# Performance work log

Hardware: AMD Instinct MI355X
Metric: run time of the kernel (lower is better)

The kernel has to match this reference:

```python
import jax, jax.numpy as jnp
import numpy as np

N, F_IN, D, H = 4096, 128, 128, 4  # nodes, in_features, n_hidden(out_features), n_heads


def setup_inputs() -> dict:
    key = jax.random.key(0)
    ks = jax.random.split(key, 5)
    h = jax.random.normal(ks[0], (N, F_IN), jnp.float32)
    adj_mat = jax.random.randint(ks[1], (N, N), 0, 2, jnp.int32)
    pos = jax.random.normal(ks[2], (N, 3), jnp.float32)
    # xavier_normal-ish scales
    W = jax.random.normal(ks[3], (F_IN, D * H), jnp.float32) * (2.0 / (F_IN + D * H)) ** 0.5
    a = jax.random.normal(ks[4], (H, 2 * D, 1), jnp.float32) * (2.0 / (2 * D + 1)) ** 0.5
    ln_gamma = jnp.ones((D,), jnp.float32)
    ln_beta = jnp.zeros((D,), jnp.float32)
    return dict(h=h, adj_mat=adj_mat, pos=pos, W=W, a=a, ln_gamma=ln_gamma, ln_beta=ln_beta)


def reference(h, adj_mat, pos, W, a, ln_gamma, ln_beta):
    n = h.shape[0]
    ht = (h @ W).reshape(n, H, D).transpose(1, 0, 2)          # (H, N, D)
    src = ht @ a[:, :D, :]                                    # (H, N, 1)
    tgt = ht @ a[:, D:, :]                                    # (H, N, 1)
    diff = pos[:, None, :] - pos[None, :, :]                  # (N, N, 3) rel_pos
    dist = jnp.sqrt(jnp.sum(diff * diff, axis=-1))            # (N, N) cdist p=2
    e = src + jnp.transpose(tgt, (0, 2, 1)) - dist[None]      # (H, N, N)
    e = jnp.where(e > 0, e, 0.2 * e)                          # LeakyReLU(0.2)
    e = jnp.where(adj_mat[None] > 0, e, jnp.float32(-9e15))   # connectivity mask
    attention = jax.nn.softmax(e, axis=-1)                    # (H, N, N)
    h_prime = attention @ ht                                  # (H, N, D)
    hm = jnp.mean(h_prime, axis=0)                            # (N, D) mean over heads
    mu = jnp.mean(hm, axis=-1, keepdims=True)
    var = jnp.var(hm, axis=-1, keepdims=True)
    hn = (hm - mu) / jnp.sqrt(var + 1e-5) * ln_gamma + ln_beta  # LayerNorm
    h_out = h + hn
    att_mean = jnp.mean(attention, axis=0)                    # (N, N)
    delta = jnp.einsum('ij,ijk->ik', att_mean, diff)          # (N, 3)
    pos_out = pos + delta
    return h_out, pos_out
```

## Files before the change

kernel.cpp:

```cpp
#include <hip/hip_runtime.h>
#include <hip/hip_bf16.h>
#include <math.h>

#define NN 4096
#define HH 4

typedef _Float16 h2 __attribute__((ext_vector_type(2)));
typedef _Float16 h4 __attribute__((ext_vector_type(4)));
typedef _Float16 h8 __attribute__((ext_vector_type(8)));
typedef float f4 __attribute__((ext_vector_type(4)));

static __device__ __forceinline__ h2 cvt2(float a, float b) {
  return __builtin_bit_cast(h2, __builtin_amdgcn_cvt_pkrtz(a, b));
}

__global__ __launch_bounds__(512) void k_htgemm(const float* __restrict__ h,
                                                const float* __restrict__ W,
                                                const float* __restrict__ a,
                                                const float* __restrict__ pos,
                                                _Float16* __restrict__ vfrag,
                                                _Float16* __restrict__ posfrag,
                                                float* __restrict__ src,
                                                float* __restrict__ tgt) {
  __shared__ float hs[16][128];
  __shared__ float red[8][16][2];
  const int jt = blockIdx.x;
  const int i0 = jt * 16;
  const int tid = threadIdx.x;
  for (int idx = tid; idx < 16 * 128; idx += 512)
    hs[idx >> 7][idx & 127] = h[(i0 + (idx >> 7)) * 128 + (idx & 127)];
  __syncthreads();
  const int c = tid;
  float acc[16];
#pragma unroll
  for (int r = 0; r < 16; ++r) acc[r] = 0.f;
  for (int k = 0; k < 128; ++k) {
    const float w = W[k * 512 + c];
#pragma unroll
    for (int r = 0; r < 16; ++r) acc[r] = fmaf(hs[r][k], w, acc[r]);
  }
  const int hc = c >> 7, d = c & 127;
  _Float16* vb = vfrag + ((size_t)(hc * 256 + jt) * 64) * 32 + (d >> 4) * 4;
#pragma unroll
  for (int rg = 0; rg < 4; ++rg) {
    h4 v;
    v.x = (_Float16)acc[rg * 4 + 0];
    v.y = (_Float16)acc[rg * 4 + 1];
    v.z = (_Float16)acc[rg * 4 + 2];
    v.w = (_Float16)acc[rg * 4 + 3];
    *(h4*)(vb + ((d & 15) + 16 * rg) * 32) = v;
  }
  const float av = a[hc * 256 + d];
  const float bvv = a[hc * 256 + 128 + d];
  float sv[16], tv[16];
#pragma unroll
  for (int r = 0; r < 16; ++r) { sv[r] = acc[r] * av; tv[r] = acc[r] * bvv; }
#pragma unroll
  for (int off = 32; off >= 1; off >>= 1) {
#pragma unroll
    for (int r = 0; r < 16; ++r) {
      sv[r] += __shfl_xor(sv[r], off, 64);
      tv[r] += __shfl_xor(tv[r], off, 64);
    }
  }
  const int w = tid >> 6;
  if ((tid & 63) == 0) {
#pragma unroll
    for (int r = 0; r < 16; ++r) { red[w][r][0] = sv[r]; red[w][r][1] = tv[r]; }
  }
  if (tid < 64) {
    const int rg = tid >> 4, n = tid & 15;
    h4 pv;
#pragma unroll
    for (int e = 0; e < 4; ++e) {
      const int j = i0 + rg * 4 + e;
      pv[e] = (_Float16)(n < 3 ? pos[j * 3 + n] : (n == 3 ? 1.f : 0.f));
    }
    *(h4*)(posfrag + (size_t)(jt * 64 + tid) * 4) = pv;
  }
  __syncthreads();
  if (tid < 128) {
    const int h2_ = tid >> 5, k = tid & 31, r = k >> 1, st = k & 1;
    const float vsum = red[h2_ * 2][r][st] + red[h2_ * 2 + 1][r][st];
    (st ? tgt : src)[h2_ * NN + i0 + r] = vsum;
  }
}

#define JROW 1036
#define SMEM_BYTES 67584

__global__ __launch_bounds__(512, 3) void k_attn(
    const _Float16* __restrict__ vfrag, const _Float16* __restrict__ posfrag,
    const int* __restrict__ adj, const float* __restrict__ pos,
    const float* __restrict__ src, const float* __restrict__ tgt,
    __hip_bfloat16* __restrict__ hp_part, __hip_bfloat16* __restrict__ ppart) {
  __shared__ __attribute__((aligned(16))) unsigned char smem[SMEM_BYTES];
  _Float16* dist16 = (_Float16*)smem;

  const int tid = threadIdx.x;
  const int bid = (int)blockIdx.x;
  const int ib = bid >> 2, jhb = bid & 3;
  const int i0 = ib * 32;
  const int jb = jhb * 1024;

  {
    const int si = tid >> 4;
    const int jc = (tid & 15) * 4;
    const float pix = pos[(i0 + si) * 3 + 0];
    const float piy = pos[(i0 + si) * 3 + 1];
    const float piz = pos[(i0 + si) * 3 + 2];
    const int* adjp = adj + (size_t)(i0 + si) * NN + jb + jc;
    const float* posj = pos + (size_t)(jb + jc) * 3;
#pragma unroll
    for (int cc = 0; cc < 16; ++cc) {
      const int4 av = *(const int4*)(adjp + cc * 64);
      const float4 p0 = *(const float4*)(posj + cc * 192 + 0);
      const float4 p1 = *(const float4*)(posj + cc * 192 + 4);
      const float4 p2 = *(const float4*)(posj + cc * 192 + 8);
      float dx, dy, dz;
      h4 dd;
      dx = pix - p0.x; dy = piy - p0.y; dz = piz - p0.z;
      dd.x = (_Float16)(av.x > 0 ? sqrtf(dx * dx + dy * dy + dz * dz) : 3e4f);
      dx = pix - p0.w; dy = piy - p1.x; dz = piz - p1.y;
      dd.y = (_Float16)(av.y > 0 ? sqrtf(dx * dx + dy * dy + dz * dz) : 3e4f);
      dx = pix - p1.z; dy = piy - p1.w; dz = piz - p2.x;
      dd.z = (_Float16)(av.z > 0 ? sqrtf(dx * dx + dy * dy + dz * dz) : 3e4f);
      dx = pix - p2.y; dy = piy - p2.z; dz = piz - p2.w;
      dd.w = (_Float16)(av.w > 0 ? sqrtf(dx * dx + dy * dy + dz * dz) : 3e4f);
      *(h4*)(dist16 + si * JROW + jc + cc * 64) = dd;
    }
  }
  __syncthreads();

  const int w = tid >> 6, lane = tid & 63;
  const int hh = w & 3, kp = w >> 2;
  const int il = lane & 15, kg = lane >> 4;

  const float srcv0 = src[hh * NN + i0 + il];
  const float srcv1 = src[hh * NN + i0 + 16 + il];

  f4 acc[2][8];
#pragma unroll
  for (int mp = 0; mp < 2; ++mp)
#pragma unroll
    for (int dt = 0; dt < 8; ++dt) acc[mp][dt] = (f4){0.f, 0.f, 0.f, 0.f};
  f4 pacc0 = (f4){0.f, 0.f, 0.f, 0.f};
  f4 pacc1 = (f4){0.f, 0.f, 0.f, 0.f};

  const int jt0 = (jb >> 4) + kp;
  const _Float16* vbase = vfrag + ((size_t)(hh * 256 + jt0) * 64 + lane) * 32;
  const _Float16* pbase = posfrag + (size_t)(jt0 * 64 + lane) * 4;
  const float* tbase = tgt + hh * NN + jb + kp * 16 + kg * 4;
  const _Float16* ddbase = dist16 + il * JROW + kp * 16 + kg * 4;

#define RELOAD(V01, V23, V45, V67, PF, TT, T)                \
  {                                                          \
    const _Float16* vfn = vbase + (size_t)(T) * 4096;        \
    V01 = *(const h8*)(vfn);                                 \
    V23 = *(const h8*)(vfn + 8);                             \
    V45 = *(const h8*)(vfn + 16);                            \
    V67 = *(const h8*)(vfn + 24);                            \
    PF = *(const h4*)(pbase + (T) * 512);                    \
    TT = *(const float4*)(tbase + (T) * 32);                 \
  }

#define BODYM(V01, V23, V45, V67, PF, TT, T)                                    \
  {                                                                             \
    const int toff = 2 * (T) * 16;                                              \
    const h4 dd0 = *(const h4*)(ddbase + toff);                                 \
    const h4 dd1 = *(const h4*)(ddbase + 16 * JROW + toff);                     \
    float e0 = (srcv0 + TT.x) - (float)dd0.x;                                   \
    float e1 = (srcv0 + TT.y) - (float)dd0.y;                                   \
    float e2 = (srcv0 + TT.z) - (float)dd0.z;                                   \
    float e3 = (srcv0 + TT.w) - (float)dd0.w;                                   \
    e0 = fmaxf(e0, 0.2f * e0); e1 = fmaxf(e1, 0.2f * e1);                       \
    e2 = fmaxf(e2, 0.2f * e2); e3 = fmaxf(e3, 0.2f * e3);                       \
    const h2 lo0 = cvt2(__expf(e0), __expf(e1));                                \
    const h2 hi0 = cvt2(__expf(e2), __expf(e3));                                \
    const h4 af0 = __builtin_shufflevector(lo0, hi0, 0, 1, 2, 3);               \
    float f0 = (srcv1 + TT.x) - (float)dd1.x;                                   \
    float f1 = (srcv1 + TT.y) - (float)dd1.y;                                   \
    float f2 = (srcv1 + TT.z) - (float)dd1.z;                                   \
    float f3 = (srcv1 + TT.w) - (float)dd1.w;                                   \
    f0 = fmaxf(f0, 0.2f * f0); f1 = fmaxf(f1, 0.2f * f1);                       \
    f2 = fmaxf(f2, 0.2f * f2); f3 = fmaxf(f3, 0.2f * f3);                       \
    const h2 lo1 = cvt2(__expf(f0), __expf(f1));                                \
    const h2 hi1 = cvt2(__expf(f2), __expf(f3));                                \
    const h4 af1 = __builtin_shufflevector(lo1, hi1, 0, 1, 2, 3);               \
    h4 vfj[8];                                                                  \
    vfj[0] = __builtin_shufflevector(V01, V01, 0, 1, 2, 3);                     \
    vfj[1] = __builtin_shufflevector(V01, V01, 4, 5, 6, 7);                     \
    vfj[2] = __builtin_shufflevector(V23, V23, 0, 1, 2, 3);                     \
    vfj[3] = __builtin_shufflevector(V23, V23, 4, 5, 6, 7);                     \
    vfj[4] = __builtin_shufflevector(V45, V45, 0, 1, 2, 3);                     \
    vfj[5] = __builtin_shufflevector(V45, V45, 4, 5, 6, 7);                     \
    vfj[6] = __builtin_shufflevector(V67, V67, 0, 1, 2, 3);                     \
    vfj[7] = __builtin_shufflevector(V67, V67, 4, 5, 6, 7);                     \
    __builtin_amdgcn_s_setprio(1);                                              \
    _Pragma("unroll") for (int dt = 0; dt < 8; ++dt)                            \
        acc[0][dt] = __builtin_amdgcn_mfma_f32_16x16x16f16(af0, vfj[dt],        \
                                                           acc[0][dt], 0, 0, 0);\
    pacc0 = __builtin_amdgcn_mfma_f32_16x16x16f16(af0, PF, pacc0, 0, 0, 0);     \
    _Pragma("unroll") for (int dt = 0; dt < 8; ++dt)                            \
        acc[1][dt] = __builtin_amdgcn_mfma_f32_16x16x16f16(af1, vfj[dt],        \
                                                           acc[1][dt], 0, 0, 0);\
    pacc1 = __builtin_amdgcn_mfma_f32_16x16x16f16(af1, PF, pacc1, 0, 0, 0);     \
    __builtin_amdgcn_s_setprio(0);                                              \
  }

  h8 A01, A23, A45, A67; h4 Apf; float4 Att;
  h8 B01, B23, B45, B67; h4 Bpf; float4 Btt;
  RELOAD(A01, A23, A45, A67, Apf, Att, 0);
  RELOAD(B01, B23, B45, B67, Bpf, Btt, 1);

#pragma unroll 1
  for (int t2 = 0; t2 < 15; ++t2) {
    const int t = t2 * 2;
    BODYM(A01, A23, A45, A67, Apf, Att, t);
    RELOAD(A01, A23, A45, A67, Apf, Att, t + 2);
    BODYM(B01, B23, B45, B67, Bpf, Btt, t + 1);
    RELOAD(B01, B23, B45, B67, Bpf, Btt, t + 3);
  }
  BODYM(A01, A23, A45, A67, Apf, Att, 30);
  BODYM(B01, B23, B45, B67, Bpf, Btt, 31);

#undef RELOAD
#undef BODYM

  __syncthreads();
  float* eps = (float*)smem;
  float* pacc_s = (float*)(smem + 65536);
  if (kp == 1) {
#pragma unroll
    for (int mp = 0; mp < 2; ++mp)
#pragma unroll
      for (int dt = 0; dt < 8; ++dt)
#pragma unroll
        for (int r = 0; r < 4; ++r)
          eps[(hh * 32 + mp * 16 + kg * 4 + r) * 128 + dt * 16 + il] = acc[mp][dt][r];
    if (il < 4) {
#pragma unroll
      for (int r = 0; r < 4; ++r) {
        pacc_s[(hh * 32 + kg * 4 + r) * 4 + il] = pacc0[r];
        pacc_s[(hh * 32 + 16 + kg * 4 + r) * 4 + il] = pacc1[r];
      }
    }
  }
  __syncthreads();
  if (kp == 0) {
    __hip_bfloat16* hpb = hp_part + ((size_t)(jhb * 4 + hh) * NN + i0) * 128;
#pragma unroll
    for (int mp = 0; mp < 2; ++mp)
#pragma unroll
      for (int dt = 0; dt < 8; ++dt)
#pragma unroll
        for (int r = 0; r < 4; ++r) {
          const int ii = mp * 16 + kg * 4 + r;
          const float s = (mp == 0 ? acc[0][dt][r] : acc[1][dt][r]) +
                          eps[(hh * 32 + ii) * 128 + dt * 16 + il];
          hpb[(size_t)ii * 128 + dt * 16 + il] = __float2bfloat16(s);
        }
    if (il < 4) {
#pragma unroll
      for (int r = 0; r < 4; ++r) {
        const float s0 = pacc0[r] + pacc_s[(hh * 32 + kg * 4 + r) * 4 + il];
        ppart[((size_t)(jhb * 4 + hh) * NN + i0 + kg * 4 + r) * 4 + il] =
            __float2bfloat16(s0);
        const float s1 = pacc1[r] + pacc_s[(hh * 32 + 16 + kg * 4 + r) * 4 + il];
        ppart[((size_t)(jhb * 4 + hh) * NN + i0 + 16 + kg * 4 + r) * 4 + il] =
            __float2bfloat16(s1);
      }
    }
  }
}

__global__ __launch_bounds__(128) void k_finish(
    const __hip_bfloat16* __restrict__ hp_part,
    const __hip_bfloat16* __restrict__ ppart, const float* __restrict__ hin,
    const float* __restrict__ pos, const float* __restrict__ gamma,
    const float* __restrict__ beta, float* __restrict__ hout,
    float* __restrict__ out_pos) {
  __shared__ float red[2][2];
  const int i = blockIdx.x, d = threadIdx.x;
  float Li[4];
  float v = 0.f;
#pragma unroll
  for (int hx = 0; hx < 4; ++hx) {
    float L = 0.f, hv = 0.f;
#pragma unroll
    for (int jh = 0; jh < 4; ++jh) {
      L += __bfloat162float(ppart[((size_t)(jh * 4 + hx) * NN + i) * 4 + 3]);
      hv += __bfloat162float(hp_part[((size_t)(jh * 4 + hx) * NN + i) * 128 + d]);
    }
    Li[hx] = 1.f / L;
    v += hv * Li[hx];
  }
  v *= 0.25f;
  float s = v, sq = v * v;
#pragma unroll
  for (int off = 32; off >= 1; off >>= 1) {
    s += __shfl_xor(s, off, 64);
    sq += __shfl_xor(sq, off, 64);
  }
  const int wv = d >> 6;
  if ((d & 63) == 0) { red[wv][0] = s; red[wv][1] = sq; }
  __syncthreads();
  s = red[0][0] + red[1][0];
  sq = red[0][1] + red[1][1];
  const float mu = s * (1.f / 128.f);
  const float var = sq * (1.f / 128.f) - mu * mu;
  const float hn = (v - mu) * rsqrtf(var + 1e-5f) * gamma[d] + beta[d];
  hout[i * 128 + d] = hin[i * 128 + d] + hn;
  if (d < 3) {
    float sp = 0.f;
#pragma unroll
    for (int hx = 0; hx < 4; ++hx) {
      float pv = 0.f;
#pragma unroll
      for (int jh = 0; jh < 4; ++jh)
        pv += __bfloat162float(ppart[((size_t)(jh * 4 + hx) * NN + i) * 4 + d]);
      sp += pv * Li[hx];
    }
    out_pos[i * 3 + d] = 2.f * pos[i * 3 + d] - 0.25f * sp;
  }
}

extern "C" void kernel_launch(void* const* d_in, const int* in_sizes, int n_in,
                              void* d_out, int out_size, void* d_ws, size_t ws_size,
                              hipStream_t stream) {
  const float* h     = (const float*)d_in[0];
  const int*   adj   = (const int*)d_in[1];
  const float* pos   = (const float*)d_in[2];
  const float* W     = (const float*)d_in[3];
  const float* a     = (const float*)d_in[4];
  const float* gamma = (const float*)d_in[5];
  const float* beta  = (const float*)d_in[6];
  float* out = (float*)d_out;

  unsigned char* ws = (unsigned char*)d_ws;
  _Float16* vfrag   = (_Float16*)ws;
  _Float16* posfrag = (_Float16*)(ws + 4194304);
  float* src        = (float*)(ws + 4194304 + 131072);
  float* tgt        = (float*)(ws + 4194304 + 131072 + 65536);
  __hip_bfloat16* hp_part =
      (__hip_bfloat16*)(ws + 4194304 + 131072 + 131072);
  __hip_bfloat16* ppart =
      (__hip_bfloat16*)(ws + 4194304 + 131072 + 131072 + 16777216);

  k_htgemm<<<NN / 16, 512, 0, stream>>>(h, W, a, pos, vfrag, posfrag, src, tgt);
  k_attn<<<(NN / 32) * 4, 512, 0, stream>>>(vfrag, posfrag, adj, pos, src, tgt,
                                            hp_part, ppart);
  k_finish<<<NN, 128, 0, stream>>>(hp_part, ppart, h, pos, gamma, beta, out,
                                   out + NN * 128);
}
```

Measured before the change: 107.8 us.

## Use exp2 with log2e prescaling, single-buffer prefetch loop, raise occupancy to 4

Multiplies src/tgt and the distances by log2(e) ahead of time so the inner loop can call the hardware exp2 directly instead of __expf, which saves a multiply per element. The two-register-set double-buffered loop becomes a single-stage prefetch loop that also prefetches the LDS distance values, which cuts register pressure. The launch bound rises from 3 to 4 blocks per CU. The masked-entry sentinel changes from 3e4 to 4e4, and the extra occupancy depends on LDS use and registers fitting; otherwise the lighter prefetch may hide less memory latency.

```diff
diff --git a/kernel.cpp b/kernel.cpp
--- a/kernel.cpp
+++ b/kernel.cpp
@@ -4,6 +4,7 @@
 
 #define NN 4096
 #define HH 4
+#define LOG2E 1.44269504f
 
 typedef _Float16 h2 __attribute__((ext_vector_type(2)));
 typedef _Float16 h4 __attribute__((ext_vector_type(4)));
@@ -13,6 +14,12 @@
 static __device__ __forceinline__ h2 cvt2(float a, float b) {
   return __builtin_bit_cast(h2, __builtin_amdgcn_cvt_pkrtz(a, b));
 }
+
+#if __has_builtin(__builtin_amdgcn_exp2f)
+#define EXP2(x) __builtin_amdgcn_exp2f(x)
+#else
+#define EXP2(x) exp2f(x)
+#endif
 
 __global__ __launch_bounds__(512) void k_htgemm(const float* __restrict__ h,
                                                 const float* __restrict__ W,
@@ -81,7 +88,7 @@
   __syncthreads();
   if (tid < 128) {
     const int h2_ = tid >> 5, k = tid & 31, r = k >> 1, st = k & 1;
-    const float vsum = red[h2_ * 2][r][st] + red[h2_ * 2 + 1][r][st];
+    const float vsum = (red[h2_ * 2][r][st] + red[h2_ * 2 + 1][r][st]) * LOG2E;
     (st ? tgt : src)[h2_ * NN + i0 + r] = vsum;
   }
 }
@@ -89,7 +96,7 @@
 #define JROW 1036
 #define SMEM_BYTES 67584
 
-__global__ __launch_bounds__(512, 3) void k_attn(
+__global__ __launch_bounds__(512, 4) void k_attn(
     const _Float16* __restrict__ vfrag, const _Float16* __restrict__ posfrag,
     const int* __restrict__ adj, const float* __restrict__ pos,
     const float* __restrict__ src, const float* __restrict__ tgt,
@@ -120,13 +127,13 @@
       float dx, dy, dz;
       h4 dd;
       dx = pix - p0.x; dy = piy - p0.y; dz = piz - p0.z;
-      dd.x = (_Float16)(av.x > 0 ? sqrtf(dx * dx + dy * dy + dz * dz) : 3e4f);
+      dd.x = (_Float16)(av.x > 0 ? sqrtf(dx * dx + dy * dy + dz * dz) * LOG2E : 4e4f);
       dx = pix - p0.w; dy = piy - p1.x; dz = piz - p1.y;
-      dd.y = (_Float16)(av.y > 0 ? sqrtf(dx * dx + dy * dy + dz * dz) : 3e4f);
+      dd.y = (_Float16)(av.y > 0 ? sqrtf(dx * dx + dy * dy + dz * dz) * LOG2E : 4e4f);
       dx = pix - p1.z; dy = piy - p1.w; dz = piz - p2.x;
-      dd.z = (_Float16)(av.z > 0 ? sqrtf(dx * dx + dy * dy + dz * dz) : 3e4f);
+      dd.z = (_Float16)(av.z > 0 ? sqrtf(dx * dx + dy * dy + dz * dz) * LOG2E : 4e4f);
       dx = pix - p2.y; dy = piy - p2.z; dz = piz - p2.w;
-      dd.w = (_Float16)(av.w > 0 ? sqrtf(dx * dx + dy * dy + dz * dz) : 3e4f);
+      dd.w = (_Float16)(av.w > 0 ? sqrtf(dx * dx + dy * dy + dz * dz) * LOG2E : 4e4f);
       *(h4*)(dist16 + si * JROW + jc + cc * 64) = dd;
     }
   }
@@ -153,79 +160,70 @@
   const float* tbase = tgt + hh * NN + jb + kp * 16 + kg * 4;
   const _Float16* ddbase = dist16 + il * JROW + kp * 16 + kg * 4;
 
-#define RELOAD(V01, V23, V45, V67, PF, TT, T)                \
-  {                                                          \
-    const _Float16* vfn = vbase + (size_t)(T) * 4096;        \
-    V01 = *(const h8*)(vfn);                                 \
-    V23 = *(const h8*)(vfn + 8);                             \
-    V45 = *(const h8*)(vfn + 16);                            \
-    V67 = *(const h8*)(vfn + 24);                            \
-    PF = *(const h4*)(pbase + (T) * 512);                    \
-    TT = *(const float4*)(tbase + (T) * 32);                 \
-  }
-
-#define BODYM(V01, V23, V45, V67, PF, TT, T)                                    \
-  {                                                                             \
-    const int toff = 2 * (T) * 16;                                              \
-    const h4 dd0 = *(const h4*)(ddbase + toff);                                 \
-    const h4 dd1 = *(const h4*)(ddbase + 16 * JROW + toff);                     \
-    float e0 = (srcv0 + TT.x) - (float)dd0.x;                                   \
-    float e1 = (srcv0 + TT.y) - (float)dd0.y;                                   \
-    float e2 = (srcv0 + TT.z) - (float)dd0.z;                                   \
-    float e3 = (srcv0 + TT.w) - (float)dd0.w;                                   \
-    e0 = fmaxf(e0, 0.2f * e0); e1 = fmaxf(e1, 0.2f * e1);                       \
-    e2 = fmaxf(e2, 0.2f * e2); e3 = fmaxf(e3, 0.2f * e3);                       \
-    const h2 lo0 = cvt2(__expf(e0), __expf(e1));                                \
-    const h2 hi0 = cvt2(__expf(e2), __expf(e3));                                \
-    const h4 af0 = __builtin_shufflevector(lo0, hi0, 0, 1, 2, 3);               \
-    float f0 = (srcv1 + TT.x) - (float)dd1.x;                                   \
-    float f1 = (srcv1 + TT.y) - (float)dd1.y;                                   \
-    float f2 = (srcv1 + TT.z) - (float)dd1.z;                                   \
-    float f3 = (srcv1 + TT.w) - (float)dd1.w;                                   \
-    f0 = fmaxf(f0, 0.2f * f0); f1 = fmaxf(f1, 0.2f * f1);                       \
-    f2 = fmaxf(f2, 0.2f * f2); f3 = fmaxf(f3, 0.2f * f3);                       \
-    const h2 lo1 = cvt2(__expf(f0), __expf(f1));                                \
-    const h2 hi1 = cvt2(__expf(f2), __expf(f3));                                \
-    const h4 af1 = __builtin_shufflevector(lo1, hi1, 0, 1, 2, 3);               \
-    h4 vfj[8];                                                                  \
-    vfj[0] = __builtin_shufflevector(V01, V01, 0, 1, 2, 3);                     \
-    vfj[1] = __builtin_shufflevector(V01, V01, 4, 5, 6, 7);                     \
-    vfj[2] = __builtin_shufflevector(V23, V23, 0, 1, 2, 3);                     \
-    vfj[3] = __builtin_shufflevector(V23, V23, 4, 5, 6, 7);                     \
-    vfj[4] = __builtin_shufflevector(V45, V45, 0, 1, 2, 3);                     \
-    vfj[5] = __builtin_shufflevector(V45, V45, 4, 5, 6, 7);                     \
-    vfj[6] = __builtin_shufflevector(V67, V67, 0, 1, 2, 3);                     \
-    vfj[7] = __builtin_shufflevector(V67, V67, 4, 5, 6, 7);                     \
-    __builtin_amdgcn_s_setprio(1);                                              \
-    _Pragma("unroll") for (int dt = 0; dt < 8; ++dt)                            \
-        acc[0][dt] = __builtin_amdgcn_mfma_f32_16x16x16f16(af0, vfj[dt],        \
-                                                           acc[0][dt], 0, 0, 0);\
-    pacc0 = __builtin_amdgcn_mfma_f32_16x16x16f16(af0, PF, pacc0, 0, 0, 0);     \
-    _Pragma("unroll") for (int dt = 0; dt < 8; ++dt)                            \
-        acc[1][dt] = __builtin_amdgcn_mfma_f32_16x16x16f16(af1, vfj[dt],        \
-                                                           acc[1][dt], 0, 0, 0);\
-    pacc1 = __builtin_amdgcn_mfma_f32_16x16x16f16(af1, PF, pacc1, 0, 0, 0);     \
-    __builtin_amdgcn_s_setprio(0);                                              \
-  }
-
-  h8 A01, A23, A45, A67; h4 Apf; float4 Att;
-  h8 B01, B23, B45, B67; h4 Bpf; float4 Btt;
-  RELOAD(A01, A23, A45, A67, Apf, Att, 0);
-  RELOAD(B01, B23, B45, B67, Bpf, Btt, 1);
-
-#pragma unroll 1
-  for (int t2 = 0; t2 < 15; ++t2) {
-    const int t = t2 * 2;
-    BODYM(A01, A23, A45, A67, Apf, Att, t);
-    RELOAD(A01, A23, A45, A67, Apf, Att, t + 2);
-    BODYM(B01, B23, B45, B67, Bpf, Btt, t + 1);
-    RELOAD(B01, B23, B45, B67, Bpf, Btt, t + 3);
-  }
-  BODYM(A01, A23, A45, A67, Apf, Att, 30);
-  BODYM(B01, B23, B45, B67, Bpf, Btt, 31);
-
-#undef RELOAD
-#undef BODYM
+  h8 n01 = *(const h8*)(vbase);
+  h8 n23 = *(const h8*)(vbase + 8);
+  h8 n45 = *(const h8*)(vbase + 16);
+  h8 n67 = *(const h8*)(vbase + 24);
+  h4 npf = *(const h4*)(pbase);
+  float4 ntt = *(const float4*)(tbase);
+  h4 ndd0 = *(const h4*)(ddbase);
+  h4 ndd1 = *(const h4*)(ddbase + 16 * JROW);
+
+#pragma unroll 2
+  for (int t = 0; t < 32; ++t) {
+    const h8 v01 = n01, v23 = n23, v45 = n45, v67 = n67;
+    const h4 pf = npf;
+    const float4 tt = ntt;
+    const h4 dd0 = ndd0, dd1 = ndd1;
+    if (t < 31) {
+      const _Float16* vfn = vbase + (size_t)(t + 1) * 4096;
+      n01 = *(const h8*)(vfn);
+      n23 = *(const h8*)(vfn + 8);
+      n45 = *(const h8*)(vfn + 16);
+      n67 = *(const h8*)(vfn + 24);
+      npf = *(const h4*)(pbase + (t + 1) * 512);
+      ntt = *(const float4*)(tbase + (t + 1) * 32);
+      ndd0 = *(const h4*)(ddbase + (t + 1) * 32);
+      ndd1 = *(const h4*)(ddbase + 16 * JROW + (t + 1) * 32);
+    }
+    float e0 = (srcv0 + tt.x) - (float)dd0.x;
+    float e1 = (srcv0 + tt.y) - (float)dd0.y;
+    float e2 = (srcv0 + tt.z) - (float)dd0.z;
+    float e3 = (srcv0 + tt.w) - (float)dd0.w;
+    e0 = fmaxf(e0, 0.2f * e0); e1 = fmaxf(e1, 0.2f * e1);
+    e2 = fmaxf(e2, 0.2f * e2); e3 = fmaxf(e3, 0.2f * e3);
+    const h2 lo0 = cvt2(EXP2(e0), EXP2(e1));
+    const h2 hi0 = cvt2(EXP2(e2), EXP2(e3));
+    const h4 af0 = __builtin_shufflevector(lo0, hi0, 0, 1, 2, 3);
+    float f0 = (srcv1 + tt.x) - (float)dd1.x;
+    float f1 = (srcv1 + tt.y) - (float)dd1.y;
+    float f2 = (srcv1 + tt.z) - (float)dd1.z;
+    float f3 = (srcv1 + tt.w) - (float)dd1.w;
+    f0 = fmaxf(f0, 0.2f * f0); f1 = fmaxf(f1, 0.2f * f1);
+    f2 = fmaxf(f2, 0.2f * f2); f3 = fmaxf(f3, 0.2f * f3);
+    const h2 lo1 = cvt2(EXP2(f0), EXP2(f1));
+    const h2 hi1 = cvt2(EXP2(f2), EXP2(f3));
+    const h4 af1 = __builtin_shufflevector(lo1, hi1, 0, 1, 2, 3);
+    h4 vfj[8];
+    vfj[0] = __builtin_shufflevector(v01, v01, 0, 1, 2, 3);
+    vfj[1] = __builtin_shufflevector(v01, v01, 4, 5, 6, 7);
+    vfj[2] = __builtin_shufflevector(v23, v23, 0, 1, 2, 3);
+    vfj[3] = __builtin_shufflevector(v23, v23, 4, 5, 6, 7);
+    vfj[4] = __builtin_shufflevector(v45, v45, 0, 1, 2, 3);
+    vfj[5] = __builtin_shufflevector(v45, v45, 4, 5, 6, 7);
+    vfj[6] = __builtin_shufflevector(v67, v67, 0, 1, 2, 3);
+    vfj[7] = __builtin_shufflevector(v67, v67, 4, 5, 6, 7);
+    __builtin_amdgcn_s_setprio(1);
+#pragma unroll
+    for (int dt = 0; dt < 8; ++dt)
+      acc[0][dt] = __builtin_amdgcn_mfma_f32_16x16x16f16(af0, vfj[dt], acc[0][dt], 0, 0, 0);
+    pacc0 = __builtin_amdgcn_mfma_f32_16x16x16f16(af0, pf, pacc0, 0, 0, 0);
+#pragma unroll
+    for (int dt = 0; dt < 8; ++dt)
+      acc[1][dt] = __builtin_amdgcn_mfma_f32_16x16x16f16(af1, vfj[dt], acc[1][dt], 0, 0, 0);
+    pacc1 = __builtin_amdgcn_mfma_f32_16x16x16f16(af1, pf, pacc1, 0, 0, 0);
+    __builtin_amdgcn_s_setprio(0);
+  }
 
   __syncthreads();
   float* eps = (float*)smem;
```

Result: slower. 137.1 us (+27.2%).
